# Performance work log

Hardware: AMD Instinct MI355X
Metric: run time of the kernel (lower is better)

Reference implementation:

```python
import jax, jax.numpy as jnp
import numpy as np

B, N, C = 8, 1024, 1024
H = 16
D = C // H  # head_dim = 64


def apply_rope(t, cos, sin):
    # t: (B,H,N,D), cos/sin: (N, D//2). Interleaved-pair RoPE
    # (matches repeat_interleave(2) + stack(-y2,y1) in the torch code).
    tr = t.reshape(*t.shape[:-1], D // 2, 2)
    t1, t2 = tr[..., 0], tr[..., 1]
    o1 = t1 * cos - t2 * sin
    o2 = t2 * cos + t1 * sin
    return jnp.stack((o1, o2), axis=-1).reshape(t.shape)


def setup_inputs() -> dict:
    key = jax.random.key(0)
    k1, k2, k3, k4 = jax.random.split(key, 4)
    s = 0.02
    x = jax.random.normal(k1, (B, N, C), dtype=jnp.float32)
    w_qkv = jax.random.normal(k2, (C, 3 * C), dtype=jnp.float32) * s  # qkv_bias=False
    w_proj = jax.random.normal(k3, (C, C), dtype=jnp.float32) * s
    b_proj = jax.random.normal(k4, (C,), dtype=jnp.float32) * s
    return {"x": x, "w_qkv": w_qkv, "w_proj": w_proj, "b_proj": b_proj}


def reference(x, w_qkv, w_proj, b_proj):
    # QKV projection: (B,N,3C) -> (3,B,H,N,D)
    qkv = (x @ w_qkv).reshape(B, N, 3, H, D).transpose(2, 0, 3, 1, 4)
    q, k, v = qkv[0], qkv[1], qkv[2]

    # RoPE tables: pos = arange(N) (mask=None, no cls/registers)
    pos = jnp.arange(N, dtype=jnp.float32)
    omega = 1.0 / (10000.0 ** (jnp.arange(D // 2, dtype=jnp.float32) / (D / 2.0)))
    freq = pos[:, None] * omega  # (N, D//2)
    cos, sin = jnp.cos(freq), jnp.sin(freq)

    q = apply_rope(q, cos, sin)
    k = apply_rope(k, cos, sin)

    # Scaled dot-product attention (non-causal, no dropout in eval)
    scale = 1.0 / jnp.sqrt(jnp.float32(D))
    scores = jnp.einsum('bhqd,bhkd->bhqk', q, k) * scale
    attn = jax.nn.softmax(scores, axis=-1)
    out = jnp.einsum('bhqk,bhkd->bhqd', attn, v)

    # Merge heads + output projection
    out = out.transpose(0, 2, 1, 3).reshape(B, N, C)
    return out @ w_proj + b_proj
```

## Files before the change

kernel.cpp:

```cpp
#include <hip/hip_runtime.h>
#include <hip/hip_bf16.h>
#include <math.h>

#define Bsz  8
#define Nseq 1024
#define Cdim 1024
#define Hh   16
#define Dd   64

typedef short short8 __attribute__((ext_vector_type(8)));
typedef float floatx4 __attribute__((ext_vector_type(4)));

__device__ __forceinline__ unsigned short f2bf(float f) {
    __hip_bfloat16 h = __float2bfloat16(f);
    return __builtin_bit_cast(unsigned short, h);
}
__device__ __forceinline__ float b2f(unsigned short u) {
    return __uint_as_float(((unsigned)u) << 16);
}

__device__ __forceinline__ void async16(const void* g, void* l) {
    __builtin_amdgcn_global_load_lds(
        (const __attribute__((address_space(1))) unsigned int*)g,
        (__attribute__((address_space(3))) unsigned int*)l, 16, 0, 0);
}

__device__ __forceinline__ unsigned pack_bf16(float lo, float hi) {
    unsigned ulo = __float_as_uint(lo) + 0x8000u;
    unsigned uhi = __float_as_uint(hi) + 0x8000u;
    return __builtin_amdgcn_perm(uhi, ulo, 0x07060302);
}

__global__ __launch_bounds__(256) void prep(
    const float* __restrict__ x, const float* __restrict__ w_qkv,
    const float* __restrict__ w_proj,
    unsigned short* __restrict__ xb, unsigned short* __restrict__ wqkvt,
    unsigned short* __restrict__ wprojt, float2* __restrict__ rope)
{
    __shared__ float T[64][65];
    const int blk = blockIdx.x;
    const int tid = threadIdx.x;

    if (blk < 8192) {
        int i = blk * 256 + tid;
        float4 v = ((const float4*)x)[i];
        ushort4 u;
        u.x = f2bf(v.x); u.y = f2bf(v.y); u.z = f2bf(v.z); u.w = f2bf(v.w);
        ((ushort4*)xb)[i] = u;
        return;
    }
    if (blk < 9216) {
        const float* in;
        unsigned short* out;
        int R = 1024, Ccols, c0, r0;
        if (blk < 8960) {
            int b2 = blk - 8192;
            in = w_qkv; out = wqkvt; Ccols = 3072;
            c0 = (b2 % 48) * 64; r0 = (b2 / 48) * 64;
        } else {
            int b2 = blk - 8960;
            in = w_proj; out = wprojt; Ccols = 1024;
            c0 = (b2 % 16) * 64; r0 = (b2 / 16) * 64;
        }
        for (int i = tid; i < 4096; i += 256) {
            int r = i >> 6, c = i & 63;
            T[r][c] = in[(size_t)(r0 + r) * Ccols + c0 + c];
        }
        __syncthreads();
        for (int i = tid; i < 4096; i += 256) {
            int rr = i >> 6, cc = i & 63;
            out[(size_t)(c0 + rr) * R + r0 + cc] = f2bf(T[cc][rr]);
        }
        return;
    }
    {
        int i = (blk - 9216) * 256 + tid;
        int n = i >> 5, p = i & 31;
        float omega = __expf(-(float)p * 0.2878231366242557f);
        float sv, cv;
        sincosf((float)n * omega, &sv, &cv);
        rope[i] = make_float2(cv, sv);
    }
}

template <int MODE>
__global__ __launch_bounds__(256) void gemm_bf16(
    const unsigned short* __restrict__ A, const unsigned short* __restrict__ Bt,
    const float* __restrict__ bias, const float2* __restrict__ rope,
    unsigned short* __restrict__ qb, unsigned short* __restrict__ kb,
    unsigned short* __restrict__ vtb, float* __restrict__ out)
{
    const int K = 1024;
    __shared__ short SM[2][128][64];
    const int tid  = threadIdx.x;
    const int wave = tid >> 6, lane = tid & 63;
    const int ml = lane & 15, quad = lane >> 4;
    const int wm = wave >> 1, wn = wave & 1;
    const int bm = blockIdx.y * 128, bn = blockIdx.x * 128;

    const int lr     = lane >> 3;
    const int lchunk = ((lane & 7) ^ lr) * 8;

    floatx4 acc[4][4] = {};

    for (int k0 = 0; k0 < K; k0 += 64) {
        #pragma unroll
        for (int t = 0; t < 4; ++t) {
            int r8  = (wave * 4 + t) * 8;
            int row = r8 + lr;
            async16(A  + (size_t)(bm + row) * K + k0 + lchunk, &SM[0][r8][0]);
            async16(Bt + (size_t)(bn + row) * K + k0 + lchunk, &SM[1][r8][0]);
        }
        __syncthreads();

        #pragma unroll
        for (int ks = 0; ks < 2; ++ks) {
            const int sl = ((ks * 4 + quad) ^ (ml & 7)) * 8;
            short8 araw[4], braw[4];
            #pragma unroll
            for (int mi = 0; mi < 4; ++mi)
                araw[mi] = *(const short8*)&SM[0][wm * 64 + mi * 16 + ml][sl];
            #pragma unroll
            for (int ni = 0; ni < 4; ++ni)
                braw[ni] = *(const short8*)&SM[1][wn * 64 + ni * 16 + ml][sl];
            #pragma unroll
            for (int mi = 0; mi < 4; ++mi)
                #pragma unroll
                for (int ni = 0; ni < 4; ++ni)
                    acc[mi][ni] = __builtin_amdgcn_mfma_f32_16x16x32_bf16(
                        araw[mi], braw[ni], acc[mi][ni], 0, 0, 0);
        }
        __syncthreads();
    }

    if (MODE == 0) {
        const int region = bn >> 10;
        const int b = bm >> 10;
        if (region < 2) {
            float2* Rs = (float2*)&SM[0][0][0];
            #pragma unroll
            for (int t = 0; t < 16; ++t) {
                int idx = t * 256 + tid;
                Rs[idx] = rope[(size_t)((bm + (idx >> 5)) & 1023) * 32 + (idx & 31)];
            }
            __syncthreads();
            unsigned short* dst = (region == 0) ? qb : kb;
            const float scale = (region == 0) ? 0.125f : 1.f;
            const float sgn = (ml & 1) ? 1.f : -1.f;
            #pragma unroll
            for (int ni = 0; ni < 4; ++ni) {
                int col = bn + wn * 64 + ni * 16 + ml;
                int jj = col & 1023;
                int h = jj >> 6, d = jj & 63;
                int p = d >> 1;
                #pragma unroll
                for (int mi = 0; mi < 4; ++mi)
                    #pragma unroll
                    for (int r = 0; r < 4; ++r) {
                        int rl = wm * 64 + mi * 16 + quad * 4 + r;
                        int n  = (bm + rl) & 1023;
                        float val = acc[mi][ni][r];
                        float partner = __shfl_xor(val, 1);
                        float2 cs = Rs[rl * 32 + p];
                        dst[(((size_t)(b * Hh + h)) * Nseq + n) * Dd + d] =
                            f2bf((val * cs.x + sgn * partner * cs.y) * scale);
                    }
            }
        } else {
            short* T = &SM[0][0][0];
            const int n0 = bm & 1023;
            #pragma unroll
            for (int hw = 0; hw < 2; ++hw) {
                if (hw) __syncthreads();
                if (wn == hw) {
                    #pragma unroll
                    for (int ni = 0; ni < 4; ++ni) {
                        int dcol = ni * 16 + ml;
                        #pragma unroll
                        for (int mi = 0; mi < 4; ++mi)
                            #pragma unroll
                            for (int r = 0; r < 4; ++r) {
                                int rl = wm * 64 + mi * 16 + quad * 4 + r;
                                T[dcol * 132 + rl] = (short)f2bf(acc[mi][ni][r]);
                            }
                    }
                }
                __syncthreads();
                int h = ((bn & 1023) >> 6) + hw;
                #pragma unroll
                for (int t = 0; t < 8; ++t) {
                    int idx4 = t * 256 + tid;
                    int d = idx4 >> 5, seg = idx4 & 31;
                    ushort4 v4 = *(const ushort4*)&T[d * 132 + seg * 4];
                    *(ushort4*)(vtb + (((size_t)(b * Hh + h)) * Dd + d) * Nseq
                                + n0 + seg * 4) = v4;
                }
            }
        }
    } else {
        #pragma unroll
        for (int ni = 0; ni < 4; ++ni) {
            int col = bn + wn * 64 + ni * 16 + ml;
            float bv = bias[col];
            #pragma unroll
            for (int mi = 0; mi < 4; ++mi)
                #pragma unroll
                for (int r = 0; r < 4; ++r) {
                    int row = bm + wm * 64 + mi * 16 + quad * 4 + r;
                    out[(size_t)row * 1024 + col] = acc[mi][ni][r] + bv;
                }
        }
    }
}

__global__ __launch_bounds__(256) void attn_flash_mfma(
    const unsigned short* __restrict__ qb, const unsigned short* __restrict__ kb,
    const unsigned short* __restrict__ vt, unsigned short* __restrict__ ao)
{
    const int bh  = blockIdx.x;
    const int qt  = blockIdx.y;
    const int tid = threadIdx.x;
    const int wave = tid >> 6, lane = tid & 63;
    const int ml = lane & 15, quad = lane >> 4;
    const int lr = lane >> 3;
    const int lc = ((lane & 7) ^ lr) * 8;

    __shared__ short Qs[128][64];
    __shared__ short Ks[64][64];
    __shared__ short Vs[64][64];
    __shared__ short Ps[4][32][72];

    const size_t hbase = (size_t)bh * (Nseq * Dd);
    const size_t vbase = (size_t)bh * 64;
    const int q0 = qt * 128;
    const int wq = wave * 32;
    const int wk = wave * 16;

    #pragma unroll
    for (int t = 0; t < 4; ++t)
        async16(qb + hbase + (size_t)(q0 + wq + t * 8 + lr) * 64 + lc, &Qs[wq + t * 8][0]);
    async16(kb + hbase + (size_t)(wk + lr) * 64 + lc,     &Ks[wk][0]);
    async16(kb + hbase + (size_t)(wk + 8 + lr) * 64 + lc, &Ks[wk + 8][0]);
    __syncthreads();

    short8 qfr[2][2];
    #pragma unroll
    for (int ks = 0; ks < 2; ++ks) {
        const int sl = ((ks * 4 + quad) ^ (ml & 7)) * 8;
        qfr[ks][0] = *(const short8*)&Qs[wq + ml][sl];
        qfr[ks][1] = *(const short8*)&Qs[wq + 16 + ml][sl];
    }

    float l0 = 0.f, l1 = 0.f;
    floatx4 o[2][4] = {};

    for (int kt = 0; kt < 16; ++kt) {
        const int k0r = kt * 64;
        async16(vt + (vbase + wk + lr) * Nseq + k0r + lc,     &Vs[wk][0]);
        async16(vt + (vbase + wk + 8 + lr) * Nseq + k0r + lc, &Vs[wk + 8][0]);

        floatx4 st[2][4] = {};
        #pragma unroll
        for (int ks = 0; ks < 2; ++ks) {
            const int sl = ((ks * 4 + quad) ^ (ml & 7)) * 8;
            #pragma unroll
            for (int kbk = 0; kbk < 4; ++kbk) {
                short8 kf = *(const short8*)&Ks[kbk * 16 + ml][sl];
                st[0][kbk] = __builtin_amdgcn_mfma_f32_16x16x32_bf16(kf, qfr[ks][0], st[0][kbk], 0, 0, 0);
                st[1][kbk] = __builtin_amdgcn_mfma_f32_16x16x32_bf16(kf, qfr[ks][1], st[1][kbk], 0, 0, 0);
            }
        }

        #pragma unroll
        for (int qg = 0; qg < 2; ++qg) {
            float lacc = 0.f;
            #pragma unroll
            for (int kbk = 0; kbk < 4; ++kbk) {
                float e0 = __expf(st[qg][kbk][0]);
                float e1 = __expf(st[qg][kbk][1]);
                float e2 = __expf(st[qg][kbk][2]);
                float e3 = __expf(st[qg][kbk][3]);
                lacc += (e0 + e1) + (e2 + e3);
                uint2 pk;
                pk.x = pack_bf16(e0, e1);
                pk.y = pack_bf16(e2, e3);
                *(uint2*)&Ps[wave][qg * 16 + ml][kbk * 16 + quad * 4] = pk;
            }
            if (qg == 0) l0 += lacc; else l1 += lacc;
        }
        __syncthreads();

        if (kt < 15) {
            const int k1r = k0r + 64;
            async16(kb + hbase + (size_t)(k1r + wk + lr) * 64 + lc,     &Ks[wk][0]);
            async16(kb + hbase + (size_t)(k1r + wk + 8 + lr) * 64 + lc, &Ks[wk + 8][0]);
        }

        #pragma unroll
        for (int ks = 0; ks < 2; ++ks) {
            const int sl = ((ks * 4 + quad) ^ (ml & 7)) * 8;
            short8 pf0 = *(const short8*)&Ps[wave][ml][ks * 32 + quad * 8];
            short8 pf1 = *(const short8*)&Ps[wave][16 + ml][ks * 32 + quad * 8];
            #pragma unroll
            for (int nt = 0; nt < 4; ++nt) {
                short8 vf = *(const short8*)&Vs[nt * 16 + ml][sl];
                o[0][nt] = __builtin_amdgcn_mfma_f32_16x16x32_bf16(pf0, vf, o[0][nt], 0, 0, 0);
                o[1][nt] = __builtin_amdgcn_mfma_f32_16x16x32_bf16(pf1, vf, o[1][nt], 0, 0, 0);
            }
        }
        if (kt < 15)
            __syncthreads();
    }

    l0 += __shfl_xor(l0, 16);
    l0 += __shfl_xor(l0, 32);
    l1 += __shfl_xor(l1, 16);
    l1 += __shfl_xor(l1, 32);

    const int b = bh >> 4, h = bh & 15;
    #pragma unroll
    for (int qg = 0; qg < 2; ++qg) {
        float lsrc = (qg == 0) ? l0 : l1;
        #pragma unroll
        for (int r = 0; r < 4; ++r) {
            float lq = __shfl(lsrc, quad * 4 + r);
            float inv = 1.f / lq;
            int q = q0 + wq + qg * 16 + quad * 4 + r;
            size_t rowbase = ((size_t)(b * Nseq + q)) * Cdim + h * Dd;
            #pragma unroll
            for (int nt = 0; nt < 4; ++nt)
                ao[rowbase + nt * 16 + ml] = f2bf(o[qg][nt][r] * inv);
        }
    }
}

extern "C" void kernel_launch(void* const* d_in, const int* in_sizes, int n_in,
                              void* d_out, int out_size, void* d_ws, size_t ws_size,
                              hipStream_t stream) {
    const float* x      = (const float*)d_in[0];
    const float* w_qkv  = (const float*)d_in[1];
    const float* w_proj = (const float*)d_in[2];
    const float* b_proj = (const float*)d_in[3];
    float* out = (float*)d_out;

    const size_t M8 = (size_t)8 * 1024 * 1024;
    unsigned short* qb     = (unsigned short*)d_ws;
    unsigned short* kb     = qb + M8;
    unsigned short* vt     = kb + M8;
    unsigned short* xb     = vt + M8;
    unsigned short* wqkvt  = xb + M8;
    unsigned short* wprojt = wqkvt + 3 * 1024 * 1024;
    float2*         rope   = (float2*)(wprojt + 1024 * 1024);
    unsigned short* aob    = xb;

    prep<<<9344, 256, 0, stream>>>(x, w_qkv, w_proj, xb, wqkvt, wprojt, rope);

    gemm_bf16<0><<<dim3(24, 64), 256, 0, stream>>>(xb, wqkvt, nullptr, rope,
                                                   qb, kb, vt, nullptr);

    attn_flash_mfma<<<dim3(128, 8), 256, 0, stream>>>(qb, kb, vt, aob);

    gemm_bf16<1><<<dim3(8, 64), 256, 0, stream>>>(aob, wprojt, b_proj, nullptr,
                                                  nullptr, nullptr, nullptr, out);
}
```

Measured before the change: 246.1 us.

## Shrink GEMM K-tile to 32 with smaller LDS and bf16 RoPE table

Halves the GEMM K-step from 64 to 32, shrinking the shared-memory staging buffers to about 17 KB and adding a launch bound that asks for 6 blocks per CU, so more workgroups can be resident. The XOR swizzle for the LDS layout is reworked to fit the 32-wide rows. The RoPE cos/sin table kept in shared memory is packed to bf16 pairs so it fits the smaller buffer. This trades twice as many barriers per K loop and lower RoPE table precision for higher occupancy.

After: 694.2 us. +182.1%, slower.

```diff
diff --git a/kernel.cpp b/kernel.cpp
--- a/kernel.cpp
+++ b/kernel.cpp
@@ -84,52 +84,53 @@
 }
 
 template <int MODE>
-__global__ __launch_bounds__(256) void gemm_bf16(
+__global__ __launch_bounds__(256, 6) void gemm_bf16(
     const unsigned short* __restrict__ A, const unsigned short* __restrict__ Bt,
     const float* __restrict__ bias, const float2* __restrict__ rope,
     unsigned short* __restrict__ qb, unsigned short* __restrict__ kb,
     unsigned short* __restrict__ vtb, float* __restrict__ out)
 {
     const int K = 1024;
-    __shared__ short SM[2][128][64];
+    __shared__ char smem[17408];
+    short (*As)[32] = (short(*)[32])smem;
+    short (*Bs)[32] = (short(*)[32])(smem + 8192);
+
     const int tid  = threadIdx.x;
     const int wave = tid >> 6, lane = tid & 63;
     const int ml = lane & 15, quad = lane >> 4;
     const int wm = wave >> 1, wn = wave & 1;
     const int bm = blockIdx.y * 128, bn = blockIdx.x * 128;
 
-    const int lr     = lane >> 3;
-    const int lchunk = ((lane & 7) ^ lr) * 8;
+    const int gchunk = ((lane & 3) ^ ((lane >> 3) & 3)) * 8;
+    const int srow   = lane >> 2;
+    const int rslot  = (quad ^ ((ml >> 1) & 3)) * 8;
 
     floatx4 acc[4][4] = {};
 
-    for (int k0 = 0; k0 < K; k0 += 64) {
-        #pragma unroll
-        for (int t = 0; t < 4; ++t) {
-            int r8  = (wave * 4 + t) * 8;
-            int row = r8 + lr;
-            async16(A  + (size_t)(bm + row) * K + k0 + lchunk, &SM[0][r8][0]);
-            async16(Bt + (size_t)(bn + row) * K + k0 + lchunk, &SM[1][r8][0]);
+    for (int k0 = 0; k0 < K; k0 += 32) {
+        #pragma unroll
+        for (int t = 0; t < 2; ++t) {
+            int r0  = wave * 16 + t * 64;
+            int row = r0 + srow;
+            int kp  = k0 + gchunk;
+            async16(A  + (size_t)(bm + row) * K + kp, &As[r0][0]);
+            async16(Bt + (size_t)(bn + row) * K + kp, &Bs[r0][0]);
         }
         __syncthreads();
 
-        #pragma unroll
-        for (int ks = 0; ks < 2; ++ks) {
-            const int sl = ((ks * 4 + quad) ^ (ml & 7)) * 8;
-            short8 araw[4], braw[4];
-            #pragma unroll
-            for (int mi = 0; mi < 4; ++mi)
-                araw[mi] = *(const short8*)&SM[0][wm * 64 + mi * 16 + ml][sl];
+        short8 araw[4], braw[4];
+        #pragma unroll
+        for (int mi = 0; mi < 4; ++mi)
+            araw[mi] = *(const short8*)&As[wm * 64 + mi * 16 + ml][rslot];
+        #pragma unroll
+        for (int ni = 0; ni < 4; ++ni)
+            braw[ni] = *(const short8*)&Bs[wn * 64 + ni * 16 + ml][rslot];
+        #pragma unroll
+        for (int mi = 0; mi < 4; ++mi)
             #pragma unroll
             for (int ni = 0; ni < 4; ++ni)
-                braw[ni] = *(const short8*)&SM[1][wn * 64 + ni * 16 + ml][sl];
-            #pragma unroll
-            for (int mi = 0; mi < 4; ++mi)
-                #pragma unroll
-                for (int ni = 0; ni < 4; ++ni)
-                    acc[mi][ni] = __builtin_amdgcn_mfma_f32_16x16x32_bf16(
-                        araw[mi], braw[ni], acc[mi][ni], 0, 0, 0);
-        }
+                acc[mi][ni] = __builtin_amdgcn_mfma_f32_16x16x32_bf16(
+                    araw[mi], braw[ni], acc[mi][ni], 0, 0, 0);
         __syncthreads();
     }
 
@@ -137,11 +138,12 @@
         const int region = bn >> 10;
         const int b = bm >> 10;
         if (region < 2) {
-            float2* Rs = (float2*)&SM[0][0][0];
+            unsigned* Rs = (unsigned*)smem;
             #pragma unroll
             for (int t = 0; t < 16; ++t) {
                 int idx = t * 256 + tid;
-                Rs[idx] = rope[(size_t)((bm + (idx >> 5)) & 1023) * 32 + (idx & 31)];
+                float2 cs = rope[(size_t)((bm + (idx >> 5)) & 1023) * 32 + (idx & 31)];
+                Rs[idx] = pack_bf16(cs.x, cs.y);
             }
             __syncthreads();
             unsigned short* dst = (region == 0) ? qb : kb;
@@ -161,13 +163,15 @@
                         int n  = (bm + rl) & 1023;
                         float val = acc[mi][ni][r];
                         float partner = __shfl_xor(val, 1);
-                        float2 cs = Rs[rl * 32 + p];
+                        unsigned cs = Rs[rl * 32 + p];
+                        float cv = b2f((unsigned short)(cs & 0xffff));
+                        float sv = b2f((unsigned short)(cs >> 16));
                         dst[(((size_t)(b * Hh + h)) * Nseq + n) * Dd + d] =
-                            f2bf((val * cs.x + sgn * partner * cs.y) * scale);
+                            f2bf((val * cv + sgn * partner * sv) * scale);
                     }
             }
         } else {
-            short* T = &SM[0][0][0];
+            short* T = (short*)smem;
             const int n0 = bm & 1023;
             #pragma unroll
             for (int hw = 0; hw < 2; ++hw) {
```
